# Kernel tuning notes

Measured on AMD Instinct MI355X. Metric: run time of the kernel, lower is better.

The kernel has to match this reference:

```python
import jax, jax.numpy as jnp
import numpy as np

B, E, D, O, K = 16384, 8, 1024, 1024, 2  # tokens, experts, d_model, output_size, top_k


def setup_inputs() -> dict:
    key = jax.random.key(0)
    kx, kl, kw = jax.random.split(key, 3)
    x = jax.random.normal(kx, (B, D), jnp.float32)
    # Sparse top-k gates: softmax over top-k logits, zeros elsewhere (the
    # structure SparseDispatcher assumes: (gates > 0) marks routed tokens).
    logits = jax.random.normal(kl, (B, E), jnp.float32)
    vals, idx = jax.lax.top_k(logits, K)              # [B,K]
    w = jax.nn.softmax(vals, axis=-1)
    gates = jnp.zeros((B, E), jnp.float32).at[jnp.arange(B)[:, None], idx].set(w)
    # Per-expert Linear weights/biases (nn.Linear(expert_sizes[i], output_size)).
    W = jax.random.normal(kw, (E, D, O), jnp.float32) / np.sqrt(D)
    b = jnp.zeros((E, O), jnp.float32)
    return {"x": x, "gates": gates, "W": W, "b": b}


def reference(x, gates, W, b):
    """MoE dispatch -> per-expert Linear -> gated combine.

    Mathematically identical to: for each expert e, gather tokens with
    gates[:, e] > 0, apply Linear_e, multiply by the gate value, and
    scatter-sum back to [B, O]. Expressed densely per expert (gate values
    are exactly zero for non-routed tokens), which keeps it jit-friendly.
    """
    out = jnp.zeros((x.shape[0], W.shape[-1]), x.dtype)
    for e in range(W.shape[0]):  # small fixed expert count
        out = out + (x @ W[e] + b[e]) * gates[:, e, None]
    return out
```

## Files before the change

kernel.cpp:

```cpp
#include <hip/hip_runtime.h>
#include <hip/hip_bf16.h>


#define TOK 16384
#define DD  1024
#define OO  1024
#define NE  8
#define NBIN 64
#define MAXT 168
#define BM  160
#define BN  128
#define BK  64

typedef __bf16 bf16x8 __attribute__((ext_vector_type(8)));
typedef float  f32x4  __attribute__((ext_vector_type(4)));

__device__ __forceinline__ unsigned short f2bf(float f) {
  unsigned u = __float_as_uint(f);
  u += 0x7fffu + ((u >> 16) & 1u);
  return (unsigned short)(u >> 16);
}

__device__ __forceinline__ void gload_lds16(const void* g, void* l) {
  __builtin_amdgcn_global_load_lds(
      (const __attribute__((address_space(1))) void*)g,
      (__attribute__((address_space(3))) void*)l, 16, 0, 0);
}

#define PREP_ROUTE_B 64
#define PREP_CVTX_B  4096
#define PREP_CVTW_B  2048

__global__ __launch_bounds__(256) void prep(
    const float* __restrict__ x, const float* __restrict__ gates,
    const float* __restrict__ W,
    unsigned short* __restrict__ xs, unsigned short* __restrict__ wtb,
    int* __restrict__ cnt, int* __restrict__ idx, float2* __restrict__ gp) {
  __shared__ float tile[64][65];
  int bid = blockIdx.x;

  if (bid < PREP_ROUTE_B) {
    int i = bid * 256 + threadIdx.x;
    int e1 = -1, e2 = -1; float g1 = 0.f, g2 = 0.f;
#pragma unroll
    for (int e = 0; e < NE; ++e) {
      float g = gates[i * NE + e];
      if (g > 0.f) { if (e1 < 0) { e1 = e; g1 = g; } else if (e2 < 0) { e2 = e; g2 = g; } }
    }
    if (e1 < 0) return;
    float r, s;
    if (e2 < 0) { e2 = e1; r = 1.f; s = 0.5f * g1; }
    else        { r = g1 / g2; s = g2; }
    int pid = e1 * NE + e2;
    int pos = atomicAdd(cnt + pid, 1);
    idx[pid * TOK + pos] = i;
    gp[(size_t)pid * TOK + pos] = make_float2(r, s);

  } else if (bid < PREP_ROUTE_B + PREP_CVTX_B) {
    size_t base = (size_t)(bid - PREP_ROUTE_B) * 1024 + threadIdx.x;
    const float4* xp = (const float4*)x;
#pragma unroll
    for (int q = 0; q < 4; ++q) {
      float4 v = xp[base + q * 256];
      alignas(8) unsigned short o4[4] = {f2bf(v.x), f2bf(v.y), f2bf(v.z), f2bf(v.w)};
      *(uint2*)(xs + (base + q * 256) * 4) = *(const uint2*)o4;
    }

  } else {
    int wb = bid - (PREP_ROUTE_B + PREP_CVTX_B);
    int e = wb >> 8, tt = wb & 255;
    int d0 = (tt >> 4) * 64, o0 = (tt & 15) * 64;
    const float* src = W + ((size_t)e << 20) + (size_t)d0 * OO + o0;
    for (int i = threadIdx.x; i < 1024; i += 256) {
      int r = i >> 4, c4 = (i & 15) * 4;
      float4 v = *(const float4*)(src + (size_t)r * OO + c4);
      tile[r][c4 + 0] = v.x; tile[r][c4 + 1] = v.y;
      tile[r][c4 + 2] = v.z; tile[r][c4 + 3] = v.w;
    }
    __syncthreads();
    unsigned short* dst = wtb + ((size_t)e << 20) + (size_t)o0 * DD + d0;
    for (int i = threadIdx.x; i < 512; i += 256) {
      int o = i >> 3, d8 = (i & 7) * 8;
      alignas(16) unsigned short w8[8];
#pragma unroll
      for (int j = 0; j < 8; ++j) w8[j] = f2bf(tile[d8 + j][o]);
      *(uint4*)(dst + (size_t)o * DD + d8) = *(const uint4*)w8;
    }
  }
}

__global__ __launch_bounds__(256) void moe_gemm(
    const unsigned short* __restrict__ xs,
    const unsigned short* __restrict__ wtb, const int* __restrict__ idx,
    const float2* __restrict__ gp, const int* __restrict__ cnt,
    const float* __restrict__ bias, float* __restrict__ out) {
  __shared__ unsigned short As[2 * BM * BK];
  __shared__ unsigned short Bs[2 * BN * BK];
  __shared__ int    rowsS[BM];
  __shared__ float2 gS[BM];
  __shared__ int    sPid, sLt, sCnt;

  if (threadIdx.x < 64) {
    int lane = threadIdx.x;
    if (lane == 0) sPid = -1;
    int c = cnt[lane];
    int n = (c + BM - 1) / BM;
    int pre = n;
#pragma unroll
    for (int o = 1; o < 64; o <<= 1) {
      int v = __shfl_up(pre, o);
      if (lane >= o) pre += v;
    }
    int lo = pre - n;
    int tb = blockIdx.x;
    if (tb >= lo && tb < pre) { sPid = lane; sLt = tb - lo; sCnt = c; }
  }
  __syncthreads();
  int pid = sPid;
  if (pid < 0) return;
  int lt = sLt, cntv = sCnt;
  int e1 = pid >> 3, e2 = pid & 7;
  int n0 = blockIdx.y * BN;

  int t = threadIdx.x, lane = t & 63, w = t >> 6;
  if (t < BM) {
    int slot = lt * BM + t;
    int tok = 0; float2 g = make_float2(0.f, 0.f);
    if (slot < cntv) { tok = idx[pid * TOK + slot]; g = gp[(size_t)pid * TOK + slot]; }
    rowsS[t] = tok; gS[t] = g;
  }
  __syncthreads();

  const unsigned short* aP[5];
  const unsigned short* bP[4];
  int csrc = ((((lane & 7)) ^ (lane >> 3)) << 3);
#pragma unroll
  for (int it = 0; it < 5; ++it) {
    int r = (w * 5 + it) * 8 + (lane >> 3);
    aP[it] = xs + (size_t)rowsS[r] * DD + csrc;
  }
#pragma unroll
  for (int it = 0; it < 4; ++it) {
    int r = (w * 4 + it) * 8 + (lane >> 3);
    bP[it] = wtb + ((size_t)e1 * OO + n0 + r) * DD + csrc;
  }
  const ptrdiff_t bAdv = (ptrdiff_t)(e2 - e1) * OO * DD;

  int wm = w >> 1, wn = w & 1;
  int hi = lane >> 4, lo = lane & 15;
  int aOff[5][2], bOff[4][2];
#pragma unroll
  for (int m = 0; m < 5; ++m) {
    int arow = wm * 80 + m * 16 + lo;
#pragma unroll
    for (int ks = 0; ks < 2; ++ks)
      aOff[m][ks] = arow * BK + ((((ks << 2) + hi) ^ (arow & 7)) << 3);
  }
#pragma unroll
  for (int n = 0; n < 4; ++n) {
    int brow = wn * 64 + n * 16 + lo;
#pragma unroll
    for (int ks = 0; ks < 2; ++ks)
      bOff[n][ks] = brow * BK + ((((ks << 2) + hi) ^ (brow & 7)) << 3);
  }

  auto STAGE = [&](int g, int buf) {
    int k0 = (g & 15) << 6;
    int aB = buf * (BM * BK), bB = buf * (BN * BK);
    const ptrdiff_t badd = (g & 16) ? bAdv : 0;
#pragma unroll
    for (int it = 0; it < 5; ++it)
      gload_lds16(aP[it] + k0, As + aB + (((w * 5) + it) << 9));
#pragma unroll
    for (int it = 0; it < 4; ++it)
      gload_lds16(bP[it] + badd + k0, Bs + bB + (((w << 2) + it) << 9));
  };

  f32x4 acc[5][4] = {};

  STAGE(0, 0);
#pragma unroll 1
  for (int g = 0; g < 32; ++g) {
    int cur = g & 1;
    __syncthreads();
    if (g < 31) STAGE(g + 1, cur ^ 1);
    int aB = cur * (BM * BK), bB = cur * (BN * BK);
#pragma unroll
    for (int ks = 0; ks < 2; ++ks) {
      bf16x8 af[5], bfr[4];
#pragma unroll
      for (int m = 0; m < 5; ++m) af[m] = *(const bf16x8*)(As + aB + aOff[m][ks]);
#pragma unroll
      for (int n = 0; n < 4; ++n) bfr[n] = *(const bf16x8*)(Bs + bB + bOff[n][ks]);
#pragma unroll
      for (int m = 0; m < 5; ++m)
#pragma unroll
        for (int n = 0; n < 4; ++n)
          acc[m][n] = __builtin_amdgcn_mfma_f32_16x16x32_bf16(af[m], bfr[n], acc[m][n], 0, 0, 0);
    }
    if (g == 15) {
#pragma unroll
      for (int m = 0; m < 5; ++m) {
        float rr[4];
#pragma unroll
        for (int j = 0; j < 4; ++j) rr[j] = gS[wm * 80 + m * 16 + hi * 4 + j].x;
#pragma unroll
        for (int n = 0; n < 4; ++n)
#pragma unroll
          for (int j = 0; j < 4; ++j) acc[m][n][j] *= rr[j];
      }
    }
  }

  const float* b1 = bias + e1 * OO;
  const float* b2 = bias + e2 * OO;
  float b1v[4], b2v[4];
#pragma unroll
  for (int n = 0; n < 4; ++n) {
    int col = n0 + wn * 64 + n * 16 + lo;
    b1v[n] = b1[col]; b2v[n] = b2[col];
  }
#pragma unroll
  for (int m = 0; m < 5; ++m) {
#pragma unroll
    for (int j = 0; j < 4; ++j) {
      int rl = wm * 80 + m * 16 + hi * 4 + j;
      int slot = lt * BM + rl;
      if (slot < cntv) {
        float2 g = gS[rl];
        float* orow = out + (size_t)rowsS[rl] * OO + n0 + wn * 64 + lo;
#pragma unroll
        for (int n = 0; n < 4; ++n)
          orow[n * 16] = g.y * (acc[m][n][j] + g.x * b1v[n] + b2v[n]);
      }
    }
  }
}

extern "C" void kernel_launch(void* const* d_in, const int* in_sizes, int n_in,
                              void* d_out, int out_size, void* d_ws, size_t ws_size,
                              hipStream_t stream) {
  const float* x     = (const float*)d_in[0];
  const float* gates = (const float*)d_in[1];
  const float* W     = (const float*)d_in[2];
  const float* bias  = (const float*)d_in[3];
  float* out = (float*)d_out;

  char* ws = (char*)d_ws;
  size_t off = 0;
  unsigned short* xs  = (unsigned short*)(ws + off); off += (size_t)TOK * DD * 2;
  unsigned short* wtb = (unsigned short*)(ws + off); off += (size_t)NE * DD * OO * 2;
  int*    idx  = (int*)(ws + off);    off += (size_t)NBIN * TOK * 4;
  float2* gp   = (float2*)(ws + off); off += (size_t)NBIN * TOK * 8;
  int*    cnt  = (int*)(ws + off);    off += NBIN * 4;
  if (ws_size < off) return;

  hipMemsetAsync(cnt, 0, NBIN * 4, stream);
  prep<<<PREP_ROUTE_B + PREP_CVTX_B + PREP_CVTW_B, 256, 0, stream>>>(
      x, gates, W, xs, wtb, cnt, idx, gp);
  dim3 gg(MAXT, OO / BN, 1);
  moe_gemm<<<gg, 256, 0, stream>>>(xs, wtb, idx, gp, cnt, bias, out);
}
```

Before: 153.3 us.

## Load B fragments directly into registers, bypassing LDS, with manual vmcnt pipelining

Weight (B) tiles are no longer staged through shared memory. Each wave issues global_load_dwordx4 straight into double-buffered register fragments in MFMA layout, while A tiles still go through LDS via global_load_lds. Explicit s_waitcnt vmcnt counts, sched_barriers and s_setprio replace __syncthreads, and launch bounds request 2 blocks per CU. The goal is to cut LDS traffic and footprint and to overlap loads with MFMA, at the cost of more VGPR pressure and redundant global loads of B across the waves that share the same columns.

```diff
diff --git a/kernel.cpp b/kernel.cpp
--- a/kernel.cpp
+++ b/kernel.cpp
@@ -14,6 +14,10 @@
 
 typedef __bf16 bf16x8 __attribute__((ext_vector_type(8)));
 typedef float  f32x4  __attribute__((ext_vector_type(4)));
+typedef int    i32x4  __attribute__((ext_vector_type(4)));
+
+union BU { i32x4 i; bf16x8 b; };
+__device__ __forceinline__ bf16x8 as_bf16x8(i32x4 v) { BU u; u.i = v; return u.b; }
 
 __device__ __forceinline__ unsigned short f2bf(float f) {
   unsigned u = __float_as_uint(f);
@@ -26,6 +30,9 @@
       (const __attribute__((address_space(1))) void*)g,
       (__attribute__((address_space(3))) void*)l, 16, 0, 0);
 }
+
+#define WAITVM(N) do { asm volatile("s_waitcnt vmcnt(" #N ")" ::: "memory"); \
+                       __builtin_amdgcn_sched_barrier(0); } while (0)
 
 #define PREP_ROUTE_B 64
 #define PREP_CVTX_B  4096
@@ -89,13 +96,12 @@
   }
 }
 
-__global__ __launch_bounds__(256) void moe_gemm(
+__global__ __launch_bounds__(256, 2) void moe_gemm(
     const unsigned short* __restrict__ xs,
     const unsigned short* __restrict__ wtb, const int* __restrict__ idx,
     const float2* __restrict__ gp, const int* __restrict__ cnt,
     const float* __restrict__ bias, float* __restrict__ out) {
   __shared__ unsigned short As[2 * BM * BK];
-  __shared__ unsigned short Bs[2 * BN * BK];
   __shared__ int    rowsS[BM];
   __shared__ float2 gS[BM];
   __shared__ int    sPid, sLt, sCnt;
@@ -132,23 +138,25 @@
   __syncthreads();
 
   const unsigned short* aP[5];
-  const unsigned short* bP[4];
-  int csrc = ((((lane & 7)) ^ (lane >> 3)) << 3);
+  int csrc = (((lane & 7) ^ (lane >> 3)) << 3);
 #pragma unroll
   for (int it = 0; it < 5; ++it) {
     int r = (w * 5 + it) * 8 + (lane >> 3);
     aP[it] = xs + (size_t)rowsS[r] * DD + csrc;
   }
-#pragma unroll
-  for (int it = 0; it < 4; ++it) {
-    int r = (w * 4 + it) * 8 + (lane >> 3);
-    bP[it] = wtb + ((size_t)e1 * OO + n0 + r) * DD + csrc;
-  }
-  const ptrdiff_t bAdv = (ptrdiff_t)(e2 - e1) * OO * DD;
 
   int wm = w >> 1, wn = w & 1;
   int hi = lane >> 4, lo = lane & 15;
-  int aOff[5][2], bOff[4][2];
+
+  const unsigned short* bGlob[4];
+#pragma unroll
+  for (int n = 0; n < 4; ++n) {
+    int brow = wn * 64 + n * 16 + lo;
+    bGlob[n] = wtb + ((size_t)e1 * OO + n0 + brow) * DD + hi * 8;
+  }
+  const ptrdiff_t bAdvE = (ptrdiff_t)(e2 - e1) * OO * DD;
+
+  int aOff[5][2];
 #pragma unroll
   for (int m = 0; m < 5; ++m) {
     int arow = wm * 80 + m * 16 + lo;
@@ -156,61 +164,88 @@
     for (int ks = 0; ks < 2; ++ks)
       aOff[m][ks] = arow * BK + ((((ks << 2) + hi) ^ (arow & 7)) << 3);
   }
-#pragma unroll
-  for (int n = 0; n < 4; ++n) {
-    int brow = wn * 64 + n * 16 + lo;
-#pragma unroll
-    for (int ks = 0; ks < 2; ++ks)
-      bOff[n][ks] = brow * BK + ((((ks << 2) + hi) ^ (brow & 7)) << 3);
-  }
-
-  auto STAGE = [&](int g, int buf) {
-    int k0 = (g & 15) << 6;
-    int aB = buf * (BM * BK), bB = buf * (BN * BK);
-    const ptrdiff_t badd = (g & 16) ? bAdv : 0;
-#pragma unroll
-    for (int it = 0; it < 5; ++it)
-      gload_lds16(aP[it] + k0, As + aB + (((w * 5) + it) << 9));
-#pragma unroll
-    for (int it = 0; it < 4; ++it)
-      gload_lds16(bP[it] + badd + k0, Bs + bB + (((w << 2) + it) << 9));
-  };
 
   f32x4 acc[5][4] = {};
-
-  STAGE(0, 0);
+  i32x4 B0[4][2], B1[4][2];
+
+#define ISSUE_AB(TN, BNXT)                                                    \
+  do {                                                                        \
+    const int tn_ = (TN);                                                     \
+    const int k0e_ = (tn_ & 15) << 6;                                         \
+    const int bufn_ = tn_ & 1;                                                \
+    _Pragma("unroll")                                                         \
+    for (int it_ = 0; it_ < 5; ++it_)                                         \
+      gload_lds16(aP[it_] + k0e_, As + bufn_ * (BM * BK) + (((w * 5) + it_) << 9)); \
+    const ptrdiff_t bo_ = k0e_ + ((tn_ >> 4) ? bAdvE : (ptrdiff_t)0);         \
+    _Pragma("unroll")                                                         \
+    for (int n_ = 0; n_ < 4; ++n_)                                            \
+      _Pragma("unroll")                                                       \
+      for (int ks_ = 0; ks_ < 2; ++ks_)                                       \
+        asm volatile("global_load_dwordx4 %0, %1, off"                        \
+                     : "=v"(BNXT[n_][ks_])                                    \
+                     : "v"(bGlob[n_] + bo_ + ks_ * 32)                        \
+                     : "memory");                                             \
+  } while (0)
+
+#define COMPUTE(T, BCUR)                                                      \
+  do {                                                                        \
+    const int aB_ = ((T) & 1) * (BM * BK);                                    \
+    __builtin_amdgcn_s_setprio(1);                                            \
+    _Pragma("unroll")                                                         \
+    for (int ks_ = 0; ks_ < 2; ++ks_) {                                       \
+      bf16x8 af_[5];                                                          \
+      _Pragma("unroll")                                                       \
+      for (int m_ = 0; m_ < 5; ++m_)                                          \
+        af_[m_] = *(const bf16x8*)(As + aB_ + aOff[m_][ks_]);                 \
+      _Pragma("unroll")                                                       \
+      for (int m_ = 0; m_ < 5; ++m_)                                          \
+        _Pragma("unroll")                                                     \
+        for (int n_ = 0; n_ < 4; ++n_)                                        \
+          acc[m_][n_] = __builtin_amdgcn_mfma_f32_16x16x32_bf16(              \
+              af_[m_], as_bf16x8(BCUR[n_][ks_]), acc[m_][n_], 0, 0, 0);       \
+    }                                                                         \
+    __builtin_amdgcn_s_setprio(0);                                            \
+  } while (0)
+
+#define STEP_FULL(T, BCUR, BNXT)                                              \
+  do {                                                                        \
+    WAITVM(8);                                                                \
+    __builtin_amdgcn_s_barrier();                                             \
+    __builtin_amdgcn_sched_barrier(0);                                        \
+    ISSUE_AB((T) + 1, BNXT);                                                  \
+    WAITVM(13);                                                               \
+    COMPUTE(T, BCUR);                                                         \
+  } while (0)
+
+#define RESCALE                                                               \
+  do {                                                                        \
+    _Pragma("unroll")                                                         \
+    for (int m_ = 0; m_ < 5; ++m_) {                                          \
+      float rr_[4];                                                           \
+      _Pragma("unroll")                                                       \
+      for (int j_ = 0; j_ < 4; ++j_)                                          \
+        rr_[j_] = gS[wm * 80 + m_ * 16 + hi * 4 + j_].x;                      \
+      _Pragma("unroll")                                                       \
+      for (int n_ = 0; n_ < 4; ++n_)                                          \
+        _Pragma("unroll")                                                     \
+        for (int j_ = 0; j_ < 4; ++j_) acc[m_][n_][j_] *= rr_[j_];            \
+    }                                                                         \
+  } while (0)
+
+  ISSUE_AB(0, B0);
+
 #pragma unroll 1
-  for (int g = 0; g < 32; ++g) {
-    int cur = g & 1;
-    __syncthreads();
-    if (g < 31) STAGE(g + 1, cur ^ 1);
-    int aB = cur * (BM * BK), bB = cur * (BN * BK);
-#pragma unroll
-    for (int ks = 0; ks < 2; ++ks) {
-      bf16x8 af[5], bfr[4];
-#pragma unroll
-      for (int m = 0; m < 5; ++m) af[m] = *(const bf16x8*)(As + aB + aOff[m][ks]);
-#pragma unroll
-      for (int n = 0; n < 4; ++n) bfr[n] = *(const bf16x8*)(Bs + bB + bOff[n][ks]);
-#pragma unroll
-      for (int m = 0; m < 5; ++m)
-#pragma unroll
-        for (int n = 0; n < 4; ++n)
-          acc[m][n] = __builtin_amdgcn_mfma_f32_16x16x32_bf16(af[m], bfr[n], acc[m][n], 0, 0, 0);
-    }
-    if (g == 15) {
-#pragma unroll
-      for (int m = 0; m < 5; ++m) {
-        float rr[4];
-#pragma unroll
-        for (int j = 0; j < 4; ++j) rr[j] = gS[wm * 80 + m * 16 + hi * 4 + j].x;
-#pragma unroll
-        for (int n = 0; n < 4; ++n)
-#pragma unroll
-          for (int j = 0; j < 4; ++j) acc[m][n][j] *= rr[j];
-      }
-    }
-  }
+  for (int g = 0; g < 30; g += 2) {
+    STEP_FULL(g, B0, B1);
+    STEP_FULL(g + 1, B1, B0);
+    if (g == 14) RESCALE;
+  }
+  STEP_FULL(30, B0, B1);
+  WAITVM(8);
+  __builtin_amdgcn_s_barrier();
+  __builtin_amdgcn_sched_barrier(0);
+  WAITVM(0);
+  COMPUTE(31, B1);
 
   const float* b1 = bias + e1 * OO;
   const float* b2 = bias + e2 * OO;
```

New measurement: 210.1 us. 37.1% more time.
